# Optimization experiments

Measured on AMD Instinct MI355X. Metric: run time of the kernel, lower is better.

The kernel has to match this reference:

```python
import jax, jax.numpy as jnp
import numpy as np

V, E, H, K, B, T = 50000, 256, 512, 12, 32, 256
START, STOP = 10, 11
NEG = -10000.0
Hd = H // 2


def _lstm(x, h0, c0, Wih, Whh, bih, bhh):
    # x: [T, B, D] -> hidden states [T, B, Hd]; PyTorch gate order i,f,g,o
    def step(carry, xt):
        h, c = carry
        g = xt @ Wih.T + bih + h @ Whh.T + bhh
        i, f, gg, o = jnp.split(g, 4, axis=-1)
        c = jax.nn.sigmoid(f) * c + jax.nn.sigmoid(i) * jnp.tanh(gg)
        h = jax.nn.sigmoid(o) * jnp.tanh(c)
        return (h, c), h
    _, hs = jax.lax.scan(step, (h0, c0), x)
    return hs


def setup_inputs() -> dict:
    key = jax.random.key(0)
    ks = jax.random.split(key, 12)
    inp = {}
    inp["sentence"] = jax.random.randint(ks[0], (B, T), 0, V, dtype=jnp.int32)
    lens = jax.random.randint(ks[1], (B,), 1, T + 1, dtype=jnp.int32)
    inp["seq_lens"] = jnp.sort(lens)[::-1]  # pack_padded requires descending
    emb = jax.random.normal(ks[2], (V, E)) * 0.05
    inp["emb"] = emb.at[0].set(0.0)  # padding_idx=0
    def lw(k):
        a, b, c, d = jax.random.split(k, 4)
        return (jax.random.normal(a, (4 * Hd, E)) * 0.05,
                jax.random.normal(b, (4 * Hd, Hd)) * 0.05,
                jax.random.normal(c, (4 * Hd,)) * 0.05,
                jax.random.normal(d, (4 * Hd,)) * 0.05)
    inp["Wih_f"], inp["Whh_f"], inp["bih_f"], inp["bhh_f"] = lw(ks[3])
    inp["Wih_b"], inp["Whh_b"], inp["bih_b"], inp["bhh_b"] = lw(ks[4])
    inp["h0"] = jax.random.normal(ks[5], (2, B, Hd))  # init_hidden uses randn
    inp["c0"] = jax.random.normal(ks[6], (2, B, Hd))
    inp["W_out"] = jax.random.normal(ks[7], (K, H)) * 0.05
    inp["b_out"] = jax.random.normal(ks[8], (K,)) * 0.05
    trans = jax.random.normal(ks[9], (K, K))
    inp["transitions"] = trans.at[START, :].set(NEG).at[:, STOP].set(NEG)
    return inp


def _features(sentence, seq_lens, emb, Wih_f, Whh_f, bih_f, bhh_f,
              Wih_b, Whh_b, bih_b, bhh_b, h0, c0, W_out, b_out):
    x = emb[sentence]                       # [B,T,E]
    t_idx = jnp.arange(T)
    # forward direction
    hf = _lstm(x.transpose(1, 0, 2), h0[0], c0[0], Wih_f, Whh_f, bih_f, bhh_f)
    hf = hf.transpose(1, 0, 2)              # [B,T,Hd]
    # backward direction: reverse each sequence within its length (packed semantics)
    rev_idx = jnp.where(t_idx[None, :] < seq_lens[:, None],
                        seq_lens[:, None] - 1 - t_idx[None, :], t_idx[None, :])  # [B,T]
    x_rev = jnp.take_along_axis(x, rev_idx[:, :, None], axis=1)
    hb_rev = _lstm(x_rev.transpose(1, 0, 2), h0[1], c0[1], Wih_b, Whh_b, bih_b, bhh_b)
    hb = jnp.take_along_axis(hb_rev.transpose(1, 0, 2), rev_idx[:, :, None], axis=1)
    hcat = jnp.concatenate([hf, hb], axis=-1)  # [B,T,H]
    return hcat @ W_out.T + b_out              # [B,T,K]


def _viterbi(feats, seq_lens, transitions):
    t_idx = jnp.arange(T)
    mask = t_idx[None, :] < seq_lens[:, None]           # [B,T]
    init = jnp.full((B, K), NEG).at[:, START].set(0.0)  # forward_var

    def vstep(fv, inputs):
        feat_t, m_t = inputs                            # [B,K], [B]
        scores = fv[:, None, :] + transitions[None, :, :]   # [B, next, prev]
        bp = jnp.argmax(scores, axis=-1)                # [B,K]
        best = jnp.max(scores, axis=-1) + feat_t
        return jnp.where(m_t[:, None], best, fv), bp

    fv, bps = jax.lax.scan(vstep, init, (feats.transpose(1, 0, 2), mask.T))
    terminal = fv + transitions[STOP][None, :]          # [B,K]
    best_last = jnp.argmax(terminal, axis=-1)           # [B]
    path_scores = jnp.take_along_axis(terminal, best_last[:, None], axis=1)[:, 0]

    def btstep(tag, inputs):
        bp_t, m_t = inputs
        pred_t = jnp.where(m_t, tag, -1)
        prev = jnp.take_along_axis(bp_t, tag[:, None], axis=1)[:, 0]
        return jnp.where(m_t, prev, tag), pred_t

    _, preds_rev = jax.lax.scan(btstep, best_last, (bps[::-1], mask.T[::-1]))
    preds = preds_rev[::-1].transpose(1, 0)             # [B,T], -1 past seq_len
    return path_scores, preds


def reference(sentence, seq_lens, emb, Wih_f, Whh_f, bih_f, bhh_f,
              Wih_b, Whh_b, bih_b, bhh_b, h0, c0, W_out, b_out, transitions):
    feats = _features(sentence, seq_lens, emb, Wih_f, Whh_f, bih_f, bhh_f,
                      Wih_b, Whh_b, bih_b, bhh_b, h0, c0, W_out, b_out)
    scores, preds = _viterbi(feats, seq_lens, transitions)
    return scores, preds
```

## Files before the change

### kernel.cpp

```cpp
#include <hip/hip_runtime.h>
#include <math.h>

#define T_ 256
#define B_ 32
#define E_ 256
#define HD_ 256
#define NG_ 1024
#define K_ 12
#define START_ 10
#define STOP_ 11
#define NEG_ -10000.0f
#define MAGICU 0x40000000u

typedef float f4_t __attribute__((ext_vector_type(4)));

__device__ __forceinline__ float sigf(float x) { return 1.0f / (1.0f + expf(-x)); }

__global__ void prep(const int* __restrict__ sent, const int* __restrict__ lens,
                     int* __restrict__ tokA, const float* __restrict__ Wf,
                     const float* __restrict__ Wb, float* __restrict__ WT,
                     float* __restrict__ hex, int* __restrict__ gcnt) {
    const int b = blockIdx.x, tid = threadIdx.x;
    if (b < 4096) {
        float4 m = make_float4(2.0f, 2.0f, 2.0f, 2.0f);
        ((float4*)hex)[b * 256 + tid] = m;
    } else if (b < 4608) {
        int b2 = b - 4096;
        int dir = b2 >> 8, k = b2 & 255, u = tid;
        const float* W = dir ? Wb : Wf;
        float4 v;
        v.x = W[(0 * HD_ + u) * HD_ + k];
        v.y = W[(1 * HD_ + u) * HD_ + k];
        v.z = W[(2 * HD_ + u) * HD_ + k];
        v.w = W[(3 * HD_ + u) * HD_ + k];
        ((float4*)(WT + ((size_t)dir * 256 + k) * NG_))[u] = v;
    } else {
        int e = (b - 4608) * 256 + tid;
        if (e < 128) gcnt[e] = 0;
        int dir = e >> 13, m = e & 8191, t = m >> 5, bb = m & 31;
        int len = lens[bb];
        int tt = dir ? (t < len ? len - 1 - t : t) : t;
        tokA[e] = sent[bb * T_ + tt];
    }
}

__global__ __launch_bounds__(512, 1) void mega(
    const float* __restrict__ emb, const int* __restrict__ tokA,
    const float* __restrict__ Wih_f, const float* __restrict__ Wih_b,
    const float* __restrict__ bih_f, const float* __restrict__ bhh_f,
    const float* __restrict__ bih_b, const float* __restrict__ bhh_b,
    const float* __restrict__ WhhT, float* __restrict__ G,
    const float* __restrict__ h0, const float* __restrict__ c0,
    const int* __restrict__ lens, float* __restrict__ hex,
    int* __restrict__ gcnt) {
    __shared__ float smem[24832];
    const int tid = threadIdx.x;

    if (blockIdx.x >= 64) {
        const int bi = blockIdx.x - 64;
        const int by = bi >> 4, sub = bi & 15;
        const int dir = sub >> 3, bx = sub & 7;
        const int n0 = bx * 128, m0 = by * 128;
        float* As = smem;
        float* Bs = smem + 1024;
        const int rs = (tid & 255) >> 1, kc = (tid & 1) * 4;
        const float* srow;
        if (tid < 256) {
            int tok = tokA[dir * 8192 + m0 + rs];
            srow = emb + (size_t)tok * E_;
        } else {
            int np = n0 + rs;
            int wrow = ((np & 3) << 8) | (np >> 2);
            srow = (dir ? Wih_b : Wih_f) + (size_t)wrow * E_;
        }
        float* Ls = (tid < 256) ? As : Bs;
        const int ty = tid >> 4, tx = tid & 15;

        float acc[4][8];
#pragma unroll
        for (int i = 0; i < 4; ++i)
#pragma unroll
            for (int j = 0; j < 8; ++j) acc[i][j] = 0.f;

        for (int k0 = 0; k0 < E_; k0 += 8) {
            float4 v = *(const float4*)(srow + k0 + kc);
            __syncthreads();
            Ls[(kc + 0) * 128 + rs] = v.x;
            Ls[(kc + 1) * 128 + rs] = v.y;
            Ls[(kc + 2) * 128 + rs] = v.z;
            Ls[(kc + 3) * 128 + rs] = v.w;
            __syncthreads();
#pragma unroll
            for (int k = 0; k < 8; ++k) {
                float4 a  = *(const float4*)&As[k * 128 + ty * 4];
                float4 b0 = *(const float4*)&Bs[k * 128 + tx * 8];
                float4 b1 = *(const float4*)&Bs[k * 128 + tx * 8 + 4];
                float af[4] = {a.x, a.y, a.z, a.w};
                float bf[8] = {b0.x, b0.y, b0.z, b0.w, b1.x, b1.y, b1.z, b1.w};
#pragma unroll
                for (int i = 0; i < 4; ++i)
#pragma unroll
                    for (int j = 0; j < 8; ++j) acc[i][j] += af[i] * bf[j];
            }
        }
        const float* bihp = dir ? bih_b : bih_f;
        const float* bhhp = dir ? bhh_b : bhh_f;
        float bias[8];
#pragma unroll
        for (int j = 0; j < 8; ++j) {
            int nn = n0 + tx * 8 + j;
            int wr = ((nn & 3) << 8) | (nn >> 2);
            bias[j] = bihp[wr] + bhhp[wr];
        }
#pragma unroll
        for (int i = 0; i < 4; ++i) {
            int m = m0 + ty * 4 + i;
            float* gp = G + ((size_t)dir * 8192 + m) * NG_ + n0 + tx * 8;
            f4_t o0, o1;
            o0.x = acc[i][0] + bias[0]; o0.y = acc[i][1] + bias[1];
            o0.z = acc[i][2] + bias[2]; o0.w = acc[i][3] + bias[3];
            o1.x = acc[i][4] + bias[4]; o1.y = acc[i][5] + bias[5];
            o1.z = acc[i][6] + bias[6]; o1.w = acc[i][7] + bias[7];
            asm volatile("global_store_dwordx4 %0, %1, off sc0 sc1" :: "v"(gp), "v"(o0) : "memory");
            asm volatile("global_store_dwordx4 %0, %1, off sc0 sc1" :: "v"(gp + 4), "v"(o1) : "memory");
        }
        asm volatile("s_waitcnt vmcnt(0)" ::: "memory");
        __syncthreads();
        if (tid == 0)
            __hip_atomic_fetch_add(gcnt + dir * 64 + by, 1, __ATOMIC_RELEASE, __HIP_MEMORY_SCOPE_AGENT);
        return;
    }

    float4* red4 = (float4*)smem;
    float4* hsA4 = (float4*)(smem + 22528);
    float4* hsB4 = (float4*)(smem + 23552);
    float4* hT4  = (float4*)(smem + 24576);

    const int wg = blockIdx.x;
    const int dir = wg >> 5, bt = (wg >> 3) & 3, ut = wg & 7;
    const int wv = tid >> 6, ln = tid & 63;
    const int upair = ln & 15;
    const int kssub = ln >> 4;
    const int ksup = wv >> 1, bh = wv & 1;
    const int ks = ksup * 4 + kssub;
    const int sb = bh * 4 + (ln & 3);
    const int sk = ksup * 64 + (ln >> 2) * 4;
    const int speer = sk >> 5;

    const int Tmax = lens[bt * 8];

    const float4* WT4 = (const float4*)(WhhT + (size_t)dir * 256 * NG_);
    const int gu_e = ut * 32 + upair * 2;
    float4 We[16], Wo[16];
#pragma unroll
    for (int j = 0; j < 16; ++j) {
        We[j] = WT4[(ks * 16 + j) * 256 + gu_e];
        Wo[j] = WT4[(ks * 16 + j) * 256 + gu_e + 1];
    }

    {
        int it = 0;
        while (__hip_atomic_load(gcnt + dir * 64, __ATOMIC_RELAXED, __HIP_MEMORY_SCOPE_AGENT) < 8) {
            __builtin_amdgcn_s_sleep(8);
            if (++it > (1 << 22)) break;
        }
    }

    const bool is_act = (ln < 32);
    float c = 0.f;
    float4 gpend = make_float4(0.f, 0.f, 0.f, 0.f);
    const float* Gd = G + (size_t)dir * 8192 * NG_;
    int gok = 1, gready = 0;
    if (is_act) {
        c = c0[(dir * B_ + bt * 8 + wv) * HD_ + ut * 32 + ln];
        gpend = ((const float4*)(Gd + (size_t)(bt * 8 + wv) * NG_))[ut * 32 + ln];
    }

    float* hexg = hex + (size_t)(dir * 4 + bt) * T_ * 2048;
    float4* hsX4 = bh ? hsB4 : hsA4;
    float* hsX = (float*)hsX4;

    f4_t pend;

    for (int t = 0; t < Tmax; ++t) {
        float4 hv;
        if (t == 0) {
            hv = *(const float4*)(h0 + (size_t)(dir * B_ + bt * 8 + sb) * HD_ + sk);
        } else if (speer == ut) {
            hv = hT4[sb * 8 + ((sk & 31) >> 2)];
        } else {
            asm volatile("s_waitcnt vmcnt(0)" ::: "memory");
            hv.x = pend.x; hv.y = pend.y; hv.z = pend.z; hv.w = pend.w;
            if (__float_as_uint(hv.x) == MAGICU || __float_as_uint(hv.y) == MAGICU ||
                __float_as_uint(hv.z) == MAGICU || __float_as_uint(hv.w) == MAGICU) {
                const float* src = hexg + (size_t)(t - 1) * 2048 + sb * 256 + sk;
                int it = 0;
                for (;;) {
                    __builtin_amdgcn_s_sleep(1);
                    float a0 = __hip_atomic_load(src + 0, __ATOMIC_RELAXED, __HIP_MEMORY_SCOPE_AGENT);
                    float a1 = __hip_atomic_load(src + 1, __ATOMIC_RELAXED, __HIP_MEMORY_SCOPE_AGENT);
                    float a2 = __hip_atomic_load(src + 2, __ATOMIC_RELAXED, __HIP_MEMORY_SCOPE_AGENT);
                    float a3 = __hip_atomic_load(src + 3, __ATOMIC_RELAXED, __HIP_MEMORY_SCOPE_AGENT);
                    if (!(__float_as_uint(a0) == MAGICU || __float_as_uint(a1) == MAGICU ||
                          __float_as_uint(a2) == MAGICU || __float_as_uint(a3) == MAGICU)) {
                        hv = make_float4(a0, a1, a2, a3); break;
                    }
                    if (++it > (1 << 22)) break;
                }
            }
        }
        hsX[(sk + 0) * 4 + (ln & 3)] = hv.x;
        hsX[(sk + 1) * 4 + (ln & 3)] = hv.y;
        hsX[(sk + 2) * 4 + (ln & 3)] = hv.z;
        hsX[(sk + 3) * 4 + (ln & 3)] = hv.w;
        asm volatile("s_waitcnt lgkmcnt(0)" ::: "memory");

        float4 ae0 = {0,0,0,0}, ae1 = {0,0,0,0}, ae2 = {0,0,0,0}, ae3 = {0,0,0,0};
        float4 ao0 = {0,0,0,0}, ao1 = {0,0,0,0}, ao2 = {0,0,0,0}, ao3 = {0,0,0,0};
#pragma unroll
        for (int j = 0; j < 16; ++j) {
            float4 h4 = hsX4[ks * 16 + j];
            float4 we = We[j], wo = Wo[j];
            ae0.x += we.x*h4.x; ae0.y += we.y*h4.x; ae0.z += we.z*h4.x; ae0.w += we.w*h4.x;
            ae1.x += we.x*h4.y; ae1.y += we.y*h4.y; ae1.z += we.z*h4.y; ae1.w += we.w*h4.y;
            ae2.x += we.x*h4.z; ae2.y += we.y*h4.z; ae2.z += we.z*h4.z; ae2.w += we.w*h4.z;
            ae3.x += we.x*h4.w; ae3.y += we.y*h4.w; ae3.z += we.z*h4.w; ae3.w += we.w*h4.w;
            ao0.x += wo.x*h4.x; ao0.y += wo.y*h4.x; ao0.z += wo.z*h4.x; ao0.w += wo.w*h4.x;
            ao1.x += wo.x*h4.y; ao1.y += wo.y*h4.y; ao1.z += wo.z*h4.y; ao1.w += wo.w*h4.y;
            ao2.x += wo.x*h4.z; ao2.y += wo.y*h4.z; ao2.z += wo.z*h4.z; ao2.w += wo.w*h4.z;
            ao3.x += wo.x*h4.w; ao3.y += wo.y*h4.w; ao3.z += wo.z*h4.w; ao3.w += wo.w*h4.w;
        }
        {
            float4* r = &red4[((wv * 4 + kssub) * 16 + upair) * 11 + kssub];
            r[0] = ae0; r[1] = ae1; r[2] = ae2; r[3] = ae3;
            r[4] = ao0; r[5] = ao1; r[6] = ao2; r[7] = ao3;
        }
        asm volatile("s_waitcnt lgkmcnt(0)\n\ts_barrier" ::: "memory");

        if (is_act) {
            const int b = wv, u = ln;
            const int bhv = b >> 2, bq = b & 3, up = u >> 1, par = u & 1;
            if (!gok) {
                const int byc = t >> 2;
                int itc = 0;
                while (__hip_atomic_load(gcnt + dir * 64 + byc, __ATOMIC_RELAXED,
                                         __HIP_MEMORY_SCOPE_AGENT) < 8) {
                    __builtin_amdgcn_s_sleep(2);
                    if (++itc > (1 << 22)) break;
                }
                const float* gsrc = Gd + ((size_t)t * B_ + bt * 8 + b) * NG_ + (size_t)(ut * 32 + u) * 4;
                f4_t tmp;
                asm volatile("global_load_dwordx4 %0, %1, off sc0 sc1\n\ts_waitcnt vmcnt(0)"
                             : "=v"(tmp) : "v"(gsrc) : "memory");
                gpend = make_float4(tmp.x, tmp.y, tmp.z, tmp.w);
            }
            float si = gpend.x, sf = gpend.y, sg = gpend.z, so = gpend.w;
#pragma unroll
            for (int kq = 0; kq < 4; ++kq)
#pragma unroll
                for (int kr = 0; kr < 4; ++kr) {
                    float4 p = red4[(((kq * 2 + bhv) * 4 + kr) * 16 + up) * 11 + kr + par * 4 + bq];
                    si += p.x; sf += p.y; sg += p.z; so += p.w;
                }
            c = sigf(sf) * c + sigf(si) * tanhf(sg);
            float h = sigf(so) * tanhf(c);
            ((float*)hT4)[b * 32 + u] = h;
            float* dst = hexg + (size_t)t * 2048 + b * 256 + ut * 32 + u;
            asm volatile("global_store_dword %0, %1, off sc0 sc1" :: "v"(dst), "v"(h) : "memory");
            if (t + 1 < Tmax) {
                const int byn = (t + 1) >> 2;
                if (byn > gready) {
                    int la = byn + 7; if (la > 63) la = 63;
                    if (__hip_atomic_load(gcnt + dir * 64 + la, __ATOMIC_RELAXED,
                                          __HIP_MEMORY_SCOPE_AGENT) >= 8) gready = la;
                    else if (__hip_atomic_load(gcnt + dir * 64 + byn, __ATOMIC_RELAXED,
                                               __HIP_MEMORY_SCOPE_AGENT) >= 8) gready = byn;
                }
                if (byn <= gready) {
                    gpend = ((const float4*)(Gd + ((size_t)(t + 1) * B_ + bt * 8 + b) * NG_))[ut * 32 + u];
                    gok = 1;
                } else gok = 0;
            }
        }
        if (t + 1 < Tmax && speer != ut) {
            const float* nsrc = hexg + (size_t)t * 2048 + sb * 256 + sk;
            asm volatile("global_load_dwordx4 %0, %1, off sc0 sc1"
                         : "=v"(pend) : "v"(nsrc) : "memory");
        }
        asm volatile("s_waitcnt lgkmcnt(0)\n\ts_barrier" ::: "memory");
    }
}

__global__ void feat_k(const float* __restrict__ hex, const int* __restrict__ lens,
                       const float* __restrict__ Wout, const float* __restrict__ bout,
                       float* __restrict__ feats) {
    int tid = threadIdx.x;
    int pl = tid / 12, k = tid % 12;
    int p = blockIdx.x * 16 + pl;
    int b = p >> 8, t = p & 255;
    int len = lens[b];
    int tr = t < len ? len - 1 - t : t;
    const float4* hf = (const float4*)(hex + ((size_t)(b >> 3) * T_ + t) * 2048 + (b & 7) * 256);
    const float4* hb = (const float4*)(hex + ((size_t)(4 + (b >> 3)) * T_ + tr) * 2048 + (b & 7) * 256);
    const float4* w0 = (const float4*)(Wout + (size_t)k * 512);
    const float4* w1 = (const float4*)(Wout + (size_t)k * 512 + 256);
    float acc = bout[k];
#pragma unroll 4
    for (int j = 0; j < 64; ++j) {
        float4 h4 = hf[j], v4 = w0[j];
        acc += h4.x * v4.x + h4.y * v4.y + h4.z * v4.z + h4.w * v4.w;
    }
#pragma unroll 4
    for (int j = 0; j < 64; ++j) {
        float4 h4 = hb[j], v4 = w1[j];
        acc += h4.x * v4.x + h4.y * v4.y + h4.z * v4.z + h4.w * v4.w;
    }
    feats[(size_t)p * K_ + k] = acc;
}

__global__ __launch_bounds__(512) void viterbi_k(
    const float* __restrict__ feats, const float* __restrict__ trans,
    const int* __restrict__ lens, float* __restrict__ out) {
    __shared__ float fv[2][B_][16];
    __shared__ float tl[K_][16];
    __shared__ unsigned char bp[T_][B_][6];
    __shared__ int best_last[B_];
    int tid = threadIdx.x;
    int b = tid >> 4, lane = tid & 15;
    if (tid < K_ * K_) tl[tid / 12][tid % 12] = trans[tid];
    if (lane < K_) fv[0][b][lane] = (lane == START_) ? 0.f : NEG_;
    __syncthreads();
    int len = lens[b];
    int pp = 0;
    float f_cur = 0.f;
    if (lane < K_) f_cur = feats[(size_t)b * T_ * K_ + lane];
    for (int t = 0; t < T_; ++t) {
        float f_nxt = 0.f;
        if (t + 1 < T_ && lane < K_) f_nxt = feats[((size_t)b * T_ + t + 1) * K_ + lane];
        if (lane < K_) {
            float best = fv[pp][b][0] + tl[lane][0];
            int argp = 0;
#pragma unroll
            for (int p = 1; p < K_; ++p) {
                float v = fv[pp][b][p] + tl[lane][p];
                if (v > best) { best = v; argp = p; }
            }
            float nb = best + f_cur;
            fv[pp ^ 1][b][lane] = (t < len) ? nb : fv[pp][b][lane];
            int other = __shfl_xor(argp, 1);
            if ((lane & 1) == 0) bp[t][b][lane >> 1] = (unsigned char)(argp | (other << 4));
        }
        __syncthreads();
        pp ^= 1;
        f_cur = f_nxt;
    }
    if (lane == 0) {
        float best = fv[pp][b][0] + tl[STOP_][0];
        int bl = 0;
#pragma unroll
        for (int p = 1; p < K_; ++p) {
            float v = fv[pp][b][p] + tl[STOP_][p];
            if (v > best) { best = v; bl = p; }
        }
        out[b] = best;
        best_last[b] = bl;
    }
    __syncthreads();
    if (lane == 0) {
        int tag = best_last[b];
        for (int t = T_ - 1; t >= 0; --t) {
            int m = (t < len);
            out[B_ + b * T_ + t] = (float)(m ? tag : -1);
            if (m) tag = (bp[t][b][tag >> 1] >> ((tag & 1) * 4)) & 15;
        }
    }
}

extern "C" void kernel_launch(void* const* d_in, const int* in_sizes, int n_in,
                              void* d_out, int out_size, void* d_ws, size_t ws_size,
                              hipStream_t stream) {
    const int*   sent  = (const int*)d_in[0];
    const int*   lens  = (const int*)d_in[1];
    const float* emb   = (const float*)d_in[2];
    const float* Wih_f = (const float*)d_in[3];
    const float* Whh_f = (const float*)d_in[4];
    const float* bih_f = (const float*)d_in[5];
    const float* bhh_f = (const float*)d_in[6];
    const float* Wih_b = (const float*)d_in[7];
    const float* Whh_b = (const float*)d_in[8];
    const float* bih_b = (const float*)d_in[9];
    const float* bhh_b = (const float*)d_in[10];
    const float* h0    = (const float*)d_in[11];
    const float* c0    = (const float*)d_in[12];
    const float* Wout  = (const float*)d_in[13];
    const float* bout  = (const float*)d_in[14];
    const float* trans = (const float*)d_in[15];
    float* out = (float*)d_out;

    char* ws = (char*)d_ws;
    int*   tokA  = (int*)ws;
    float* WhhT  = (float*)(ws + 65536);
    float* G     = (float*)(ws + 2162688);
    float* feats = (float*)(ws + 69271552);
    float* hex   = (float*)(ws + 69664768);
    int*   gcnt  = (int*)feats;

    prep<<<4672, 256, 0, stream>>>(sent, lens, tokA, Whh_f, Whh_b, WhhT, hex, gcnt);
    mega<<<1088, 512, 0, stream>>>(emb, tokA, Wih_f, Wih_b, bih_f, bhh_f, bih_b, bhh_b,
                                   WhhT, G, h0, c0, lens, hex, gcnt);
    feat_k<<<512, 192, 0, stream>>>(hex, lens, Wout, bout, feats);
    viterbi_k<<<1, 512, 0, stream>>>(feats, trans, lens, out);
}
```

Before: 1.112 ms.

## Fuse emission projection into mega kernel, polling hidden states as they arrive

Removes the separate feat_k launch and adds 256 extra blocks to the persistent mega kernel. Each block spin-waits on the hex buffer's sentinel values until the LSTM recurrence has written the needed hidden states, then computes the K emission scores. This overlaps the output projection with the recurrence and saves one kernel launch. The gcnt counters move into the output buffer so that feats can be written concurrently. The cost is extra polling traffic, the risk of occupying CUs the recurrence blocks need (if they are not yet resident this could deadlock), and a bounded spin loop.

After: 1.103 ms. About the same (-0.8%).

```diff
diff --git a/kernel.cpp b/kernel.cpp
--- a/kernel.cpp
+++ b/kernel.cpp
@@ -24,6 +24,7 @@
     if (b < 4096) {
         float4 m = make_float4(2.0f, 2.0f, 2.0f, 2.0f);
         ((float4*)hex)[b * 256 + tid] = m;
+        if (b == 0 && tid < 128) gcnt[tid] = 0;
     } else if (b < 4608) {
         int b2 = b - 4096;
         int dir = b2 >> 8, k = b2 & 255, u = tid;
@@ -36,7 +37,6 @@
         ((float4*)(WT + ((size_t)dir * 256 + k) * NG_))[u] = v;
     } else {
         int e = (b - 4608) * 256 + tid;
-        if (e < 128) gcnt[e] = 0;
         int dir = e >> 13, m = e & 8191, t = m >> 5, bb = m & 31;
         int len = lens[bb];
         int tt = dir ? (t < len ? len - 1 - t : t) : t;
@@ -52,9 +52,66 @@
     const float* __restrict__ WhhT, float* __restrict__ G,
     const float* __restrict__ h0, const float* __restrict__ c0,
     const int* __restrict__ lens, float* __restrict__ hex,
-    int* __restrict__ gcnt) {
+    int* __restrict__ gcnt, const float* __restrict__ Wout,
+    const float* __restrict__ bout, float* __restrict__ feats) {
     __shared__ float smem[24832];
     const int tid = threadIdx.x;
+
+    if (blockIdx.x >= 1088) {
+        const int blk = blockIdx.x - 1088;
+        f4_t* hbuf = (f4_t*)smem;
+#pragma unroll
+        for (int i = 0; i < 8; ++i) {
+            int idx = i * 512 + tid;
+            int pl = idx >> 7, j = idx & 127;
+            int p = blk * 32 + pl;
+            int b = p >> 8, t = p & 255;
+            int len = lens[b];
+            int g = b >> 3;
+            int Tg = lens[g * 8];
+            const float* addr;
+            if (j < 64) {
+                addr = hex + ((size_t)g * T_ + t) * 2048 + (b & 7) * 256 + j * 4;
+            } else {
+                int tr = t < len ? len - 1 - t : t;
+                addr = hex + ((size_t)(4 + g) * T_ + tr) * 2048 + (b & 7) * 256 + (j - 64) * 4;
+            }
+            float a0 = __hip_atomic_load(addr + 0, __ATOMIC_RELAXED, __HIP_MEMORY_SCOPE_AGENT);
+            float a1 = __hip_atomic_load(addr + 1, __ATOMIC_RELAXED, __HIP_MEMORY_SCOPE_AGENT);
+            float a2 = __hip_atomic_load(addr + 2, __ATOMIC_RELAXED, __HIP_MEMORY_SCOPE_AGENT);
+            float a3 = __hip_atomic_load(addr + 3, __ATOMIC_RELAXED, __HIP_MEMORY_SCOPE_AGENT);
+            if (t < Tg) {
+                int it = 0;
+                while (__float_as_uint(a0) == MAGICU || __float_as_uint(a1) == MAGICU ||
+                       __float_as_uint(a2) == MAGICU || __float_as_uint(a3) == MAGICU) {
+                    __builtin_amdgcn_s_sleep(2);
+                    a0 = __hip_atomic_load(addr + 0, __ATOMIC_RELAXED, __HIP_MEMORY_SCOPE_AGENT);
+                    a1 = __hip_atomic_load(addr + 1, __ATOMIC_RELAXED, __HIP_MEMORY_SCOPE_AGENT);
+                    a2 = __hip_atomic_load(addr + 2, __ATOMIC_RELAXED, __HIP_MEMORY_SCOPE_AGENT);
+                    a3 = __hip_atomic_load(addr + 3, __ATOMIC_RELAXED, __HIP_MEMORY_SCOPE_AGENT);
+                    if (++it > (1 << 22)) break;
+                }
+            }
+            f4_t v; v.x = a0; v.y = a1; v.z = a2; v.w = a3;
+            hbuf[pl * 129 + j] = v;
+        }
+        __syncthreads();
+        if (tid < 384) {
+            int pl = tid / 12, k = tid - pl * 12;
+            int p = blk * 32 + pl;
+            const float4* w0 = (const float4*)(Wout + (size_t)k * 512);
+            const f4_t* hrow = hbuf + pl * 129;
+            float acc = bout[k];
+#pragma unroll 4
+            for (int j = 0; j < 128; ++j) {
+                f4_t h4 = hrow[j];
+                float4 v4 = w0[j];
+                acc += h4.x * v4.x + h4.y * v4.y + h4.z * v4.z + h4.w * v4.w;
+            }
+            feats[(size_t)p * K_ + k] = acc;
+        }
+        return;
+    }
 
     if (blockIdx.x >= 64) {
         const int bi = blockIdx.x - 64;
@@ -127,7 +184,8 @@
         asm volatile("s_waitcnt vmcnt(0)" ::: "memory");
         __syncthreads();
         if (tid == 0)
-            __hip_atomic_fetch_add(gcnt + dir * 64 + by, 1, __ATOMIC_RELEASE, __HIP_MEMORY_SCOPE_AGENT);
+            __hip_atomic_fetch_add(gcnt + dir * 64 + by, 1,
+                                   __ATOMIC_RELEASE, __HIP_MEMORY_SCOPE_AGENT);
         return;
     }
 
@@ -291,33 +349,6 @@
     }
 }
 
-__global__ void feat_k(const float* __restrict__ hex, const int* __restrict__ lens,
-                       const float* __restrict__ Wout, const float* __restrict__ bout,
-                       float* __restrict__ feats) {
-    int tid = threadIdx.x;
-    int pl = tid / 12, k = tid % 12;
-    int p = blockIdx.x * 16 + pl;
-    int b = p >> 8, t = p & 255;
-    int len = lens[b];
-    int tr = t < len ? len - 1 - t : t;
-    const float4* hf = (const float4*)(hex + ((size_t)(b >> 3) * T_ + t) * 2048 + (b & 7) * 256);
-    const float4* hb = (const float4*)(hex + ((size_t)(4 + (b >> 3)) * T_ + tr) * 2048 + (b & 7) * 256);
-    const float4* w0 = (const float4*)(Wout + (size_t)k * 512);
-    const float4* w1 = (const float4*)(Wout + (size_t)k * 512 + 256);
-    float acc = bout[k];
-#pragma unroll 4
-    for (int j = 0; j < 64; ++j) {
-        float4 h4 = hf[j], v4 = w0[j];
-        acc += h4.x * v4.x + h4.y * v4.y + h4.z * v4.z + h4.w * v4.w;
-    }
-#pragma unroll 4
-    for (int j = 0; j < 64; ++j) {
-        float4 h4 = hb[j], v4 = w1[j];
-        acc += h4.x * v4.x + h4.y * v4.y + h4.z * v4.z + h4.w * v4.w;
-    }
-    feats[(size_t)p * K_ + k] = acc;
-}
-
 __global__ __launch_bounds__(512) void viterbi_k(
     const float* __restrict__ feats, const float* __restrict__ trans,
     const int* __restrict__ lens, float* __restrict__ out) {
@@ -403,11 +434,10 @@
     float* G     = (float*)(ws + 2162688);
     float* feats = (float*)(ws + 69271552);
     float* hex   = (float*)(ws + 69664768);
-    int*   gcnt  = (int*)feats;
+    int*   gcnt  = (int*)(out + 32);
 
     prep<<<4672, 256, 0, stream>>>(sent, lens, tokA, Whh_f, Whh_b, WhhT, hex, gcnt);
-    mega<<<1088, 512, 0, stream>>>(emb, tokA, Wih_f, Wih_b, bih_f, bhh_f, bih_b, bhh_b,
-                                   WhhT, G, h0, c0, lens, hex, gcnt);
-    feat_k<<<512, 192, 0, stream>>>(hex, lens, Wout, bout, feats);
+    mega<<<1344, 512, 0, stream>>>(emb, tokA, Wih_f, Wih_b, bih_f, bhh_f, bih_b, bhh_b,
+                                   WhhT, G, h0, c0, lens, hex, gcnt, Wout, bout, feats);
     viterbi_k<<<1, 512, 0, stream>>>(feats, trans, lens, out);
 }
```
